# Optimization experiments

Hardware: AMD Instinct MI355X
Metric: run time of the kernel (lower is better)

The kernel has to match this reference:

```python
import jax, jax.numpy as jnp
import numpy as np

N = 50000       # nodes
E = 800000      # edges (before self-loops)
G = 512         # graphs in batch
IN = 128        # in_channels
HID = 256       # hidden_channels
HEADS = 8
CH = HID // HEADS
NEG_SLOPE = 0.2 # GATConv leaky relu slope
BN_EPS = 1e-5
OUT_CLASSES = [3, 3]


def setup_inputs() -> dict:
    key = jax.random.key(0)
    ks = iter(jax.random.split(key, 64))
    inp = {}
    inp["x"] = jax.random.normal(next(ks), (N, IN), jnp.float32)
    inp["edge_index"] = jax.random.randint(next(ks), (2, E), 0, N)
    inp["batch"] = jnp.sort(jax.random.randint(next(ks), (N,), 0, G))
    dims = [IN, HID, HID]
    for l, d in enumerate(dims, start=1):
        inp[f"W{l}"] = jax.random.normal(next(ks), (d, HID), jnp.float32) / np.float32(np.sqrt(d))
        inp[f"as{l}"] = jax.random.normal(next(ks), (HEADS, CH), jnp.float32) * 0.1
        inp[f"ad{l}"] = jax.random.normal(next(ks), (HEADS, CH), jnp.float32) * 0.1
        inp[f"b{l}"] = jnp.zeros((HID,), jnp.float32)
        inp[f"g{l}"] = 1.0 + 0.1 * jax.random.normal(next(ks), (HID,), jnp.float32)
        inp[f"be{l}"] = 0.1 * jax.random.normal(next(ks), (HID,), jnp.float32)
        inp[f"m{l}"] = 0.1 * jax.random.normal(next(ks), (HID,), jnp.float32)
        inp[f"v{l}"] = 0.5 + jax.random.uniform(next(ks), (HID,), jnp.float32)
    for i, c in enumerate(OUT_CLASSES):
        inp[f"ow{i}"] = jax.random.normal(next(ks), (3 * HID, c), jnp.float32) / np.float32(np.sqrt(3 * HID))
        inp[f"ob{i}"] = jnp.zeros((c,), jnp.float32)
    return inp


def gat_conv(x, W, a_src, a_dst, bias, src, dst):
    # x: [N, D] -> h: [N, H, C]
    h = (x @ W).reshape(N, HEADS, CH)
    s_src = jnp.sum(h * a_src, axis=-1)           # [N, H]
    s_dst = jnp.sum(h * a_dst, axis=-1)           # [N, H]
    alpha = jax.nn.leaky_relu(s_src[src] + s_dst[dst], NEG_SLOPE)  # [E', H]
    # segment softmax over incoming edges of each destination node
    mx = jax.ops.segment_max(alpha, dst, num_segments=N)           # [N, H]
    e = jnp.exp(alpha - mx[dst])
    Z = jax.ops.segment_sum(e, dst, num_segments=N)                # [N, H]
    coef = e / (Z[dst] + 1e-16)                                    # [E', H]
    msg = h[src] * coef[:, :, None]                                # [E', H, C]
    out = jax.ops.segment_sum(msg, dst, num_segments=N)            # [N, H, C]
    return out.reshape(N, HID) + bias


def batch_norm(h, g, b, m, v):
    return (h - m) * jax.lax.rsqrt(v + BN_EPS) * g + b


def reference(x, edge_index, batch,
              W1, as1, ad1, b1, g1, be1, m1, v1,
              W2, as2, ad2, b2, g2, be2, m2, v2,
              W3, as3, ad3, b3, g3, be3, m3, v3,
              ow0, ob0, ow1, ob1):
    # GATConv adds self-loops by default
    loop = jnp.arange(N, dtype=edge_index.dtype)
    src = jnp.concatenate([edge_index[0], loop])
    dst = jnp.concatenate([edge_index[1], loop])

    h = jax.nn.elu(batch_norm(gat_conv(x, W1, as1, ad1, b1, src, dst), g1, be1, m1, v1))
    h = jax.nn.elu(batch_norm(gat_conv(h, W2, as2, ad2, b2, src, dst), g2, be2, m2, v2) + h)
    h = jax.nn.elu(batch_norm(gat_conv(h, W3, as3, ad3, b3, src, dst), g3, be3, m3, v3) + h)

    sums = jax.ops.segment_sum(h, batch, num_segments=G)                       # add pool
    cnt = jax.ops.segment_sum(jnp.ones((N, 1), h.dtype), batch, num_segments=G)
    mean = sums / jnp.maximum(cnt, 1.0)                                        # mean pool
    mx = jax.ops.segment_max(h, batch, num_segments=G)                         # max pool
    mx = jnp.where(jnp.isfinite(mx), mx, 0.0)
    pooled = jnp.concatenate([mean, sums, mx], axis=1)                         # [G, 3*HID]

    return (pooled @ ow0 + ob0, pooled @ ow1 + ob1)
```

## Files before the change

kernel.cpp:

```cpp
#include <hip/hip_runtime.h>
#include <hip/hip_bf16.h>
#include <math.h>

#define N_NODES 50000
#define N_EDGES 800000
#define EP (N_EDGES + N_NODES)
#define G_GRAPHS 512
#define HID 256
#define HEADS 8
#define NEG_SLOPE 0.2f
#define BN_EPS 1e-5f
#define NB_SCAN ((N_NODES + 1023) / 1024)

typedef __attribute__((ext_vector_type(8))) short short8;
typedef __attribute__((ext_vector_type(8))) unsigned short ushort8v;
typedef __attribute__((ext_vector_type(4))) float floatx4;

__device__ __forceinline__ float bf2f(ushort u) {
    return __uint_as_float(((unsigned)u) << 16);
}
__device__ __forceinline__ ushort f2bf(float f) {
    unsigned u = __float_as_uint(f);
    u += 0x7fff + ((u >> 16) & 1);
    return (ushort)(u >> 16);
}


__global__ void hist_kernel(const int* __restrict__ ei, int* __restrict__ fill) {
    int e = blockIdx.x * 256 + threadIdx.x;
    if (e >= EP) return;
    int d = (e < N_EDGES) ? ei[N_EDGES + e] : (e - N_EDGES);
    atomicAdd(&fill[d], 1);
}

__global__ void scan1_kernel(const int* __restrict__ fill, int* __restrict__ rowptr,
                             int* __restrict__ bsum) {
    __shared__ int sdata[1024];
    int tid = threadIdx.x;
    int idx = blockIdx.x * 1024 + tid;
    int v = (idx < N_NODES) ? fill[idx] : 0;
    sdata[tid] = v;
    __syncthreads();
    for (int off = 1; off < 1024; off <<= 1) {
        int x = (tid >= off) ? sdata[tid - off] : 0;
        __syncthreads();
        sdata[tid] += x;
        __syncthreads();
    }
    if (idx < N_NODES) rowptr[idx] = sdata[tid] - v;
    if (tid == 1023) bsum[blockIdx.x] = sdata[1023];
}

__global__ void scan3_kernel(int* __restrict__ rowptr, int* __restrict__ fill,
                             const int* __restrict__ bsum) {
    __shared__ int soff[2];
    int tid = threadIdx.x;
    if (tid < 64) {
        int v = (tid < NB_SCAN) ? bsum[tid] : 0;
        int incl = v;
#pragma unroll
        for (int off = 1; off < 64; off <<= 1) {
            int x = __shfl_up(incl, off, 64);
            if (tid >= off) incl += x;
        }
        if (tid == blockIdx.x) soff[0] = incl - v;
        if (tid == NB_SCAN - 1) soff[1] = incl;
    }
    __syncthreads();
    int idx = blockIdx.x * 1024 + tid;
    if (idx < N_NODES) {
        int e = rowptr[idx] + soff[0];
        rowptr[idx] = e;
        fill[idx] = e;
    }
    if (idx == N_NODES) rowptr[N_NODES] = soff[1];
}

__global__ void scatter_kernel(const int* __restrict__ ei, int* __restrict__ fill,
                               int* __restrict__ esrc) {
    int e = blockIdx.x * 256 + threadIdx.x;
    if (e >= EP) return;
    int s, d;
    if (e < N_EDGES) { s = ei[e]; d = ei[N_EDGES + e]; }
    else             { s = d = e - N_EDGES; }
    int pos = atomicAdd(&fill[d], 1);
    esrc[pos] = s;
}

__global__ void gstart_kernel(const int* __restrict__ batch, int* __restrict__ gstart) {
    int g = blockIdx.x * 64 + threadIdx.x;
    if (g > G_GRAPHS) return;
    int lo = 0, hi = N_NODES;
    while (lo < hi) { int mid = (lo + hi) >> 1; if (batch[mid] < g) lo = mid + 1; else hi = mid; }
    gstart[g] = lo;
}


__global__ void cvt_kernel(const float* __restrict__ in, ushort* __restrict__ out, int n4) {
    int i = blockIdx.x * 256 + threadIdx.x;
    if (i >= n4) return;
    float4 v = *(const float4*)&in[(size_t)i * 4];
    ushort4 o = {f2bf(v.x), f2bf(v.y), f2bf(v.z), f2bf(v.w)};
    *(ushort4*)&out[(size_t)i * 4] = o;
}

__global__ void wt_all_kernel(const float* __restrict__ W0, const float* __restrict__ W1,
                              const float* __restrict__ W2, ushort* __restrict__ Wt0,
                              ushort* __restrict__ Wt1, ushort* __restrict__ Wt2) {
    int m = blockIdx.y;
    const float* W = (m == 0) ? W0 : (m == 1) ? W1 : W2;
    ushort* Wt = (m == 0) ? Wt0 : (m == 1) ? Wt1 : Wt2;
    int K = (m == 0) ? 128 : 256;
    int c = blockIdx.x, k = threadIdx.x;
    if (k < K) Wt[(size_t)c * K + k] = f2bf(W[(size_t)k * HID + c]);
}

#define BM 128
#define BN 128
#define BK 64

__global__ __launch_bounds__(256) void gemm_kernel(
    const ushort* __restrict__ A, const ushort* __restrict__ Bt,
    ushort* __restrict__ C, int M, int K)
{
    __shared__ __align__(16) char As[2][BM * BK * 2];
    __shared__ __align__(16) char Bs[2][BN * BK * 2];

    int t = threadIdx.x;
    int w = t >> 6, lane = t & 63;
    int bm = blockIdx.x * BM, bn = blockIdx.y * BN;
    int wr = (w >> 1) * 64, wc = (w & 1) * 64;

    floatx4 acc[4][4] = {};

    int l8 = lane >> 3;
    int cb = ((lane & 7) << 4) ^ ((l8 & 7) << 4);
    int rsw = (lane & 7) << 4;
    int nt = K / BK;

    auto stage = [&](int buf, int k0) {
#pragma unroll
        for (int c = 0; c < 4; c++) {
            int q = w * 4 + c;
            int row = q * 8 + l8;
            int ar = bm + row; if (ar > M - 1) ar = M - 1;
            const char* src = (const char*)A + ((size_t)ar * K + k0) * 2 + cb;
            __builtin_amdgcn_global_load_lds(
                (const __attribute__((address_space(1))) void*)src,
                (__attribute__((address_space(3))) void*)&As[buf][q * 1024], 16, 0, 0);
            int br = bn + row;
            const char* srcb = (const char*)Bt + ((size_t)br * K + k0) * 2 + cb;
            __builtin_amdgcn_global_load_lds(
                (const __attribute__((address_space(1))) void*)srcb,
                (__attribute__((address_space(3))) void*)&Bs[buf][q * 1024], 16, 0, 0);
        }
    };

    stage(0, 0);
    for (int tt = 0; tt < nt; tt++) {
        int cur = tt & 1;
        __builtin_amdgcn_s_barrier();
        if (tt + 1 < nt) {
            stage(cur ^ 1, (tt + 1) * BK);
            asm volatile("s_waitcnt vmcnt(8)" ::: "memory");
        } else {
            asm volatile("s_waitcnt vmcnt(0)" ::: "memory");
        }
        __builtin_amdgcn_sched_barrier(0);
        __builtin_amdgcn_s_barrier();
        __builtin_amdgcn_sched_barrier(0);

        const char* asb = As[cur];
        const char* bsb = Bs[cur];
#pragma unroll
        for (int ks = 0; ks < 2; ks++) {
            int kb = ks * 64 + ((lane >> 4) << 4);
            short8 a[4], b[4];
#pragma unroll
            for (int m = 0; m < 4; m++) {
                int row = wr + m * 16 + (lane & 15);
                a[m] = *(const short8*)&asb[row * 128 + (kb ^ rsw)];
            }
#pragma unroll
            for (int n = 0; n < 4; n++) {
                int row = wc + n * 16 + (lane & 15);
                b[n] = *(const short8*)&bsb[row * 128 + (kb ^ rsw)];
            }
#pragma unroll
            for (int m = 0; m < 4; m++)
#pragma unroll
                for (int n = 0; n < 4; n++)
                    acc[m][n] = __builtin_amdgcn_mfma_f32_16x16x32_bf16(a[m], b[n], acc[m][n], 0, 0, 0);
        }
    }

    int cl = lane & 15, rh = lane >> 4;
#pragma unroll
    for (int m = 0; m < 4; m++) {
#pragma unroll
        for (int r = 0; r < 4; r++) {
            int row = bm + wr + m * 16 + rh * 4 + r;
            if (row < M) {
                size_t base = (size_t)row * HID + bn + wc;
#pragma unroll
                for (int n = 0; n < 4; n++)
                    C[base + n * 16 + cl] = f2bf(acc[m][n][r]);
            }
        }
    }
}

__global__ __launch_bounds__(256) void score_kernel(
    const ushort* __restrict__ hb, const float* __restrict__ asrc,
    const float* __restrict__ adst, float* __restrict__ ssrc,
    float* __restrict__ sdst) {
    int t = threadIdx.x;
    int lane = t & 63;
    int wid = t >> 6;
    unsigned n = (unsigned)(blockIdx.x * 8 + wid * 2 + (lane >> 5));
    unsigned cl = lane & 31;
    unsigned c0 = cl * 8u;
    ushort8v hv = *(const ushort8v*)&hb[n * 256u + c0];
    float s1 = 0.f, s2 = 0.f;
#pragma unroll
    for (int j = 0; j < 8; j++) {
        float v = bf2f(hv[j]);
        s1 += v * asrc[c0 + j];
        s2 += v * adst[c0 + j];
    }
    s1 += __shfl_xor(s1, 1, 64); s2 += __shfl_xor(s2, 1, 64);
    s1 += __shfl_xor(s1, 2, 64); s2 += __shfl_xor(s2, 2, 64);
    if ((cl & 3) == 0) {
        unsigned h = cl >> 2;
        ssrc[n * 8u + h] = s1;
        sdst[n * 8u + h] = s2;
    }
}

__global__ __launch_bounds__(256) void agg_kernel(
    const ushort* __restrict__ hb, const float* __restrict__ ssrc,
    const float* __restrict__ sdst, const int* __restrict__ rowptr,
    const int* __restrict__ esrc, const float* __restrict__ bias,
    const float* __restrict__ gam, const float* __restrict__ bet,
    const float* __restrict__ bmean, const float* __restrict__ bvar,
    const ushort* __restrict__ residb, ushort* __restrict__ outb) {
    int wid = threadIdx.x >> 6;
    int lane = threadIdx.x & 63;
    int n = blockIdx.x * 4 + wid;
    if (n >= N_NODES) return;
    int start = rowptr[n], end = rowptr[n + 1];
    int slot = lane >> 5;
    unsigned cl = lane & 31;
    unsigned c0 = cl * 8u;
    unsigned head = cl >> 2;
    float sdh = sdst[(unsigned)n * 8u + head];

    float z = 0.f;
    float acc[8] = {};
    int i = start + slot;
    for (; i + 6 < end; i += 8) {
        unsigned s0 = (unsigned)esrc[i], s1 = (unsigned)esrc[i + 2];
        unsigned s2 = (unsigned)esrc[i + 4], s3 = (unsigned)esrc[i + 6];
        float a0 = ssrc[s0 * 8u + head] + sdh;
        float a1 = ssrc[s1 * 8u + head] + sdh;
        float a2 = ssrc[s2 * 8u + head] + sdh;
        float a3 = ssrc[s3 * 8u + head] + sdh;
        ushort8v h0 = *(const ushort8v*)&hb[s0 * 256u + c0];
        ushort8v h1 = *(const ushort8v*)&hb[s1 * 256u + c0];
        ushort8v h2 = *(const ushort8v*)&hb[s2 * 256u + c0];
        ushort8v h3 = *(const ushort8v*)&hb[s3 * 256u + c0];
        a0 = fmaxf(a0, NEG_SLOPE * a0);
        a1 = fmaxf(a1, NEG_SLOPE * a1);
        a2 = fmaxf(a2, NEG_SLOPE * a2);
        a3 = fmaxf(a3, NEG_SLOPE * a3);
        float e0 = __expf(a0), e1 = __expf(a1), e2 = __expf(a2), e3 = __expf(a3);
        z += (e0 + e1) + (e2 + e3);
#pragma unroll
        for (int j = 0; j < 8; j++)
            acc[j] += (e0 * bf2f(h0[j]) + e1 * bf2f(h1[j])) +
                      (e2 * bf2f(h2[j]) + e3 * bf2f(h3[j]));
    }
    for (; i < end; i += 2) {
        unsigned s = (unsigned)esrc[i];
        float a = ssrc[s * 8u + head] + sdh;
        a = fmaxf(a, NEG_SLOPE * a);
        float e = __expf(a);
        ushort8v hv = *(const ushort8v*)&hb[s * 256u + c0];
        z += e;
#pragma unroll
        for (int j = 0; j < 8; j++)
            acc[j] += e * bf2f(hv[j]);
    }
    z += __shfl_xor(z, 32, 64);
#pragma unroll
    for (int j = 0; j < 8; j++)
        acc[j] += __shfl_xor(acc[j], 32, 64);

    if (lane < 32) {
        float inv = 1.f / (z + 1e-16f);
        float4 bv0 = *(const float4*)&bias[c0],   bv1 = *(const float4*)&bias[c0 + 4];
        float4 gv0 = *(const float4*)&gam[c0],    gv1 = *(const float4*)&gam[c0 + 4];
        float4 be0 = *(const float4*)&bet[c0],    be1 = *(const float4*)&bet[c0 + 4];
        float4 mv0 = *(const float4*)&bmean[c0],  mv1 = *(const float4*)&bmean[c0 + 4];
        float4 vv0 = *(const float4*)&bvar[c0],   vv1 = *(const float4*)&bvar[c0 + 4];
        float bs[8] = {bv0.x, bv0.y, bv0.z, bv0.w, bv1.x, bv1.y, bv1.z, bv1.w};
        float gs[8] = {gv0.x, gv0.y, gv0.z, gv0.w, gv1.x, gv1.y, gv1.z, gv1.w};
        float bes[8] = {be0.x, be0.y, be0.z, be0.w, be1.x, be1.y, be1.z, be1.w};
        float ms[8] = {mv0.x, mv0.y, mv0.z, mv0.w, mv1.x, mv1.y, mv1.z, mv1.w};
        float vs[8] = {vv0.x, vv0.y, vv0.z, vv0.w, vv1.x, vv1.y, vv1.z, vv1.w};
        float rs[8] = {};
        if (residb) {
            ushort8v rv = *(const ushort8v*)&residb[(unsigned)n * 256u + c0];
#pragma unroll
            for (int j = 0; j < 8; j++) rs[j] = bf2f(rv[j]);
        }
        ushort8v ob;
#pragma unroll
        for (int j = 0; j < 8; j++) {
            float val = acc[j] * inv + bs[j];
            val = (val - ms[j]) * rsqrtf(vs[j] + BN_EPS) * gs[j] + bes[j];
            val += rs[j];
            val = (val > 0.f) ? val : expm1f(val);
            ob[j] = f2bf(val);
        }
        *(ushort8v*)&outb[(unsigned)n * 256u + c0] = ob;
    }
}

__global__ void poolhead_kernel(const ushort* __restrict__ hbf, const int* __restrict__ gstart,
                                const float* __restrict__ ow0, const float* __restrict__ ob0,
                                const float* __restrict__ ow1, const float* __restrict__ ob1,
                                float* __restrict__ out) {
    int g = blockIdx.x;
    int t = threadIdx.x;
    int s = gstart[g], e = gstart[g + 1];
    float sum = 0.f, mx = -INFINITY;
    for (int n = s; n < e; n++) {
        float v = bf2f(hbf[(unsigned)n * 256u + t]);
        sum += v;
        mx = fmaxf(mx, v);
    }
    int cnt = e - s;
    float mean = sum / fmaxf((float)cnt, 1.f);
    if (cnt == 0) mx = 0.f;

    float a0[3], a1[3];
#pragma unroll
    for (int j = 0; j < 3; j++) {
        a0[j] = mean * ow0[t * 3 + j] + sum * ow0[(256 + t) * 3 + j] + mx * ow0[(512 + t) * 3 + j];
        a1[j] = mean * ow1[t * 3 + j] + sum * ow1[(256 + t) * 3 + j] + mx * ow1[(512 + t) * 3 + j];
    }
    __shared__ float sd[6][256];
#pragma unroll
    for (int j = 0; j < 3; j++) { sd[j][t] = a0[j]; sd[3 + j][t] = a1[j]; }
    __syncthreads();
    for (int off = 128; off; off >>= 1) {
        if (t < off) {
#pragma unroll
            for (int j = 0; j < 6; j++) sd[j][t] += sd[j][t + off];
        }
        __syncthreads();
    }
    if (t < 3) {
        out[g * 3 + t] = sd[t][0] + ob0[t];
        out[1536 + g * 3 + t] = sd[3 + t][0] + ob1[t];
    }
}

extern "C" void kernel_launch(void* const* d_in, const int* in_sizes, int n_in,
                              void* d_out, int out_size, void* d_ws, size_t ws_size,
                              hipStream_t stream) {
    const float* x     = (const float*)d_in[0];
    const int*   ei    = (const int*)d_in[1];
    const int*   batch = (const int*)d_in[2];
    const float* W[3]  = {(const float*)d_in[3], (const float*)d_in[11], (const float*)d_in[19]};
    const float* AS[3] = {(const float*)d_in[4], (const float*)d_in[12], (const float*)d_in[20]};
    const float* AD[3] = {(const float*)d_in[5], (const float*)d_in[13], (const float*)d_in[21]};
    const float* B[3]  = {(const float*)d_in[6], (const float*)d_in[14], (const float*)d_in[22]};
    const float* GM[3] = {(const float*)d_in[7], (const float*)d_in[15], (const float*)d_in[23]};
    const float* BE[3] = {(const float*)d_in[8], (const float*)d_in[16], (const float*)d_in[24]};
    const float* M[3]  = {(const float*)d_in[9], (const float*)d_in[17], (const float*)d_in[25]};
    const float* V[3]  = {(const float*)d_in[10], (const float*)d_in[18], (const float*)d_in[26]};
    const float* ow0 = (const float*)d_in[27];
    const float* ob0 = (const float*)d_in[28];
    const float* ow1 = (const float*)d_in[29];
    const float* ob1 = (const float*)d_in[30];
    float* out = (float*)d_out;

    char* p = (char*)d_ws;
    int* rowptr = (int*)p;  p += (size_t)(N_NODES + 1) * 4;
    int* fill   = (int*)p;  p += (size_t)N_NODES * 4;
    int* esrc   = (int*)p;  p += (size_t)EP * 4;
    int* gstart = (int*)p;  p += (size_t)(G_GRAPHS + 1) * 4;
    int* bsum   = (int*)p;  p += (size_t)(NB_SCAN + 1) * 4;
    p = (char*)(((uintptr_t)p + 255) & ~(uintptr_t)255);
    ushort* hb    = (ushort*)p; p += (size_t)N_NODES * HID * 2;
    ushort* curhb = (ushort*)p; p += (size_t)N_NODES * HID * 2;
    ushort* xb    = (ushort*)p; p += (size_t)N_NODES * 128 * 2;
    ushort* Wt0   = (ushort*)p; p += (size_t)256 * 128 * 2;
    ushort* Wt1   = (ushort*)p; p += (size_t)256 * 256 * 2;
    ushort* Wt2   = (ushort*)p; p += (size_t)256 * 256 * 2;
    float* ssrc   = (float*)p;  p += (size_t)N_NODES * HEADS * 4;
    float* sdst   = (float*)p;  p += (size_t)N_NODES * HEADS * 4;

    hipMemsetAsync(fill, 0, (size_t)N_NODES * 4, stream);
    hist_kernel<<<(EP + 255) / 256, 256, 0, stream>>>(ei, fill);
    scan1_kernel<<<NB_SCAN, 1024, 0, stream>>>(fill, rowptr, bsum);
    scan3_kernel<<<NB_SCAN, 1024, 0, stream>>>(rowptr, fill, bsum);
    scatter_kernel<<<(EP + 255) / 256, 256, 0, stream>>>(ei, fill, esrc);
    gstart_kernel<<<(G_GRAPHS + 64) / 64, 64, 0, stream>>>(batch, gstart);

    cvt_kernel<<<(N_NODES * 128 / 4 + 255) / 256, 256, 0, stream>>>(x, xb, N_NODES * 128 / 4);
    {
        dim3 wgrid(256, 3);
        wt_all_kernel<<<wgrid, 256, 0, stream>>>(W[0], W[1], W[2], Wt0, Wt1, Wt2);
    }
    const ushort* Wt[3] = {Wt0, Wt1, Wt2};

    dim3 ggrid((N_NODES + BM - 1) / BM, HID / BN);
    int sgrid = N_NODES / 8;
    int agrid = (N_NODES + 3) / 4;

    gemm_kernel<<<ggrid, 256, 0, stream>>>(xb, Wt[0], hb, N_NODES, 128);
    score_kernel<<<sgrid, 256, 0, stream>>>(hb, AS[0], AD[0], ssrc, sdst);
    agg_kernel<<<agrid, 256, 0, stream>>>(hb, ssrc, sdst, rowptr, esrc,
                                          B[0], GM[0], BE[0], M[0], V[0],
                                          nullptr, curhb);
    for (int l = 1; l < 3; l++) {
        gemm_kernel<<<ggrid, 256, 0, stream>>>(curhb, Wt[l], hb, N_NODES, 256);
        score_kernel<<<sgrid, 256, 0, stream>>>(hb, AS[l], AD[l], ssrc, sdst);
        agg_kernel<<<agrid, 256, 0, stream>>>(hb, ssrc, sdst, rowptr, esrc,
                                              B[l], GM[l], BE[l], M[l], V[l],
                                              curhb, curhb);
    }

    poolhead_kernel<<<G_GRAPHS, 256, 0, stream>>>(curhb, gstart, ow0, ob0, ow1, ob1, out);
}
```

Before: 561.4 us.

## Fuse attention scores into GEMM epilogue and merge preprocessing kernels

Computes the per-head source and destination attention scores inside the GEMM epilogue from fp32 accumulators. Partial dot products are reduced with wave shuffles and atomically added into zeroed per-layer score buffers, which removes the separate score kernel and its re-read of h. Also merges the bf16 conversion, weight transpose, degree histogram and graph-start search into one launch. In exchange it adds atomics, a larger memset, and scores taken from fp32 rather than bf16-rounded values.

Measured after the change: 646.3 us. 15.1% more time.

```diff
diff --git a/kernel.cpp b/kernel.cpp
--- a/kernel.cpp
+++ b/kernel.cpp
@@ -12,6 +12,12 @@
 #define BN_EPS 1e-5f
 #define NB_SCAN ((N_NODES + 1023) / 1024)
 
+#define NB_CVT 6250
+#define NB_WT  256
+#define NB_HIST ((EP + 255) / 256)
+#define NB_GST 3
+#define NB_PREP (NB_CVT + NB_WT + NB_HIST + NB_GST)
+
 typedef __attribute__((ext_vector_type(8))) short short8;
 typedef __attribute__((ext_vector_type(8))) unsigned short ushort8v;
 typedef __attribute__((ext_vector_type(4))) float floatx4;
@@ -25,12 +31,39 @@
     return (ushort)(u >> 16);
 }
 
-
-__global__ void hist_kernel(const int* __restrict__ ei, int* __restrict__ fill) {
-    int e = blockIdx.x * 256 + threadIdx.x;
-    if (e >= EP) return;
-    int d = (e < N_EDGES) ? ei[N_EDGES + e] : (e - N_EDGES);
-    atomicAdd(&fill[d], 1);
+__global__ __launch_bounds__(256) void prep_kernel(
+    const float* __restrict__ x, ushort* __restrict__ xb,
+    const float* __restrict__ W0, const float* __restrict__ W1,
+    const float* __restrict__ W2, ushort* __restrict__ Wt0,
+    ushort* __restrict__ Wt1, ushort* __restrict__ Wt2,
+    const int* __restrict__ ei, int* __restrict__ fill,
+    const int* __restrict__ batch, int* __restrict__ gstart) {
+    int b = blockIdx.x;
+    int tid = threadIdx.x;
+    if (b < NB_CVT) {
+        int i = b * 256 + tid;
+        float4 v = *(const float4*)&x[(size_t)i * 4];
+        ushort4 o = {f2bf(v.x), f2bf(v.y), f2bf(v.z), f2bf(v.w)};
+        *(ushort4*)&xb[(size_t)i * 4] = o;
+    } else if (b < NB_CVT + NB_WT) {
+        int c = b - NB_CVT;
+        if (tid < 128) Wt0[c * 128 + tid] = f2bf(W0[(size_t)tid * HID + c]);
+        Wt1[c * 256 + tid] = f2bf(W1[(size_t)tid * HID + c]);
+        Wt2[c * 256 + tid] = f2bf(W2[(size_t)tid * HID + c]);
+    } else if (b < NB_CVT + NB_WT + NB_HIST) {
+        int e = (b - NB_CVT - NB_WT) * 256 + tid;
+        if (e < EP) {
+            int d = (e < N_EDGES) ? ei[N_EDGES + e] : (e - N_EDGES);
+            atomicAdd(&fill[d], 1);
+        }
+    } else {
+        int g = (b - NB_CVT - NB_WT - NB_HIST) * 256 + tid;
+        if (g <= G_GRAPHS) {
+            int lo = 0, hi = N_NODES;
+            while (lo < hi) { int mid = (lo + hi) >> 1; if (batch[mid] < g) lo = mid + 1; else hi = mid; }
+            gstart[g] = lo;
+        }
+    }
 }
 
 __global__ void scan1_kernel(const int* __restrict__ fill, int* __restrict__ rowptr,
@@ -87,41 +120,15 @@
     esrc[pos] = s;
 }
 
-__global__ void gstart_kernel(const int* __restrict__ batch, int* __restrict__ gstart) {
-    int g = blockIdx.x * 64 + threadIdx.x;
-    if (g > G_GRAPHS) return;
-    int lo = 0, hi = N_NODES;
-    while (lo < hi) { int mid = (lo + hi) >> 1; if (batch[mid] < g) lo = mid + 1; else hi = mid; }
-    gstart[g] = lo;
-}
-
-
-__global__ void cvt_kernel(const float* __restrict__ in, ushort* __restrict__ out, int n4) {
-    int i = blockIdx.x * 256 + threadIdx.x;
-    if (i >= n4) return;
-    float4 v = *(const float4*)&in[(size_t)i * 4];
-    ushort4 o = {f2bf(v.x), f2bf(v.y), f2bf(v.z), f2bf(v.w)};
-    *(ushort4*)&out[(size_t)i * 4] = o;
-}
-
-__global__ void wt_all_kernel(const float* __restrict__ W0, const float* __restrict__ W1,
-                              const float* __restrict__ W2, ushort* __restrict__ Wt0,
-                              ushort* __restrict__ Wt1, ushort* __restrict__ Wt2) {
-    int m = blockIdx.y;
-    const float* W = (m == 0) ? W0 : (m == 1) ? W1 : W2;
-    ushort* Wt = (m == 0) ? Wt0 : (m == 1) ? Wt1 : Wt2;
-    int K = (m == 0) ? 128 : 256;
-    int c = blockIdx.x, k = threadIdx.x;
-    if (k < K) Wt[(size_t)c * K + k] = f2bf(W[(size_t)k * HID + c]);
-}
-
 #define BM 128
 #define BN 128
 #define BK 64
 
 __global__ __launch_bounds__(256) void gemm_kernel(
     const ushort* __restrict__ A, const ushort* __restrict__ Bt,
-    ushort* __restrict__ C, int M, int K)
+    ushort* __restrict__ C, int M, int K,
+    const float* __restrict__ asf, const float* __restrict__ adf,
+    float* __restrict__ ssrc, float* __restrict__ sdst)
 {
     __shared__ __align__(16) char As[2][BM * BK * 2];
     __shared__ __align__(16) char Bs[2][BN * BK * 2];
@@ -208,32 +215,38 @@
             }
         }
     }
-}
-
-__global__ __launch_bounds__(256) void score_kernel(
-    const ushort* __restrict__ hb, const float* __restrict__ asrc,
-    const float* __restrict__ adst, float* __restrict__ ssrc,
-    float* __restrict__ sdst) {
-    int t = threadIdx.x;
-    int lane = t & 63;
-    int wid = t >> 6;
-    unsigned n = (unsigned)(blockIdx.x * 8 + wid * 2 + (lane >> 5));
-    unsigned cl = lane & 31;
-    unsigned c0 = cl * 8u;
-    ushort8v hv = *(const ushort8v*)&hb[n * 256u + c0];
-    float s1 = 0.f, s2 = 0.f;
-#pragma unroll
-    for (int j = 0; j < 8; j++) {
-        float v = bf2f(hv[j]);
-        s1 += v * asrc[c0 + j];
-        s2 += v * adst[c0 + j];
-    }
-    s1 += __shfl_xor(s1, 1, 64); s2 += __shfl_xor(s2, 1, 64);
-    s1 += __shfl_xor(s1, 2, 64); s2 += __shfl_xor(s2, 2, 64);
-    if ((cl & 3) == 0) {
-        unsigned h = cl >> 2;
-        ssrc[n * 8u + h] = s1;
-        sdst[n * 8u + h] = s2;
+
+    int base_c = bn + wc;
+    float av[4], dv[4];
+#pragma unroll
+    for (int n = 0; n < 4; n++) {
+        av[n] = asf[base_c + n * 16 + cl];
+        dv[n] = adf[base_c + n * 16 + cl];
+    }
+    int headA = base_c >> 5, headB = headA + 1;
+#pragma unroll
+    for (int m = 0; m < 4; m++) {
+#pragma unroll
+        for (int r = 0; r < 4; r++) {
+            int row = bm + wr + m * 16 + rh * 4 + r;
+            float psA = acc[m][0][r] * av[0] + acc[m][1][r] * av[1];
+            float psB = acc[m][2][r] * av[2] + acc[m][3][r] * av[3];
+            float pdA = acc[m][0][r] * dv[0] + acc[m][1][r] * dv[1];
+            float pdB = acc[m][2][r] * dv[2] + acc[m][3][r] * dv[3];
+#pragma unroll
+            for (int off = 1; off < 16; off <<= 1) {
+                psA += __shfl_xor(psA, off, 64);
+                psB += __shfl_xor(psB, off, 64);
+                pdA += __shfl_xor(pdA, off, 64);
+                pdB += __shfl_xor(pdB, off, 64);
+            }
+            if (cl == 0 && row < M) {
+                atomicAdd(&ssrc[(unsigned)row * 8u + headA], psA);
+                atomicAdd(&ssrc[(unsigned)row * 8u + headB], psB);
+                atomicAdd(&sdst[(unsigned)row * 8u + headA], pdA);
+                atomicAdd(&sdst[(unsigned)row * 8u + headB], pdB);
+            }
+        }
     }
 }
 
@@ -388,8 +401,14 @@
     float* out = (float*)d_out;
 
     char* p = (char*)d_ws;
+    int* fill   = (int*)p;  p += (size_t)N_NODES * 4;
+    float* sc[3][2];
+    for (int l = 0; l < 3; l++) {
+        sc[l][0] = (float*)p; p += (size_t)N_NODES * HEADS * 4;
+        sc[l][1] = (float*)p; p += (size_t)N_NODES * HEADS * 4;
+    }
+    size_t zero_bytes = (size_t)p - (size_t)d_ws;
     int* rowptr = (int*)p;  p += (size_t)(N_NODES + 1) * 4;
-    int* fill   = (int*)p;  p += (size_t)N_NODES * 4;
     int* esrc   = (int*)p;  p += (size_t)EP * 4;
     int* gstart = (int*)p;  p += (size_t)(G_GRAPHS + 1) * 4;
     int* bsum   = (int*)p;  p += (size_t)(NB_SCAN + 1) * 4;
@@ -400,36 +419,28 @@
     ushort* Wt0   = (ushort*)p; p += (size_t)256 * 128 * 2;
     ushort* Wt1   = (ushort*)p; p += (size_t)256 * 256 * 2;
     ushort* Wt2   = (ushort*)p; p += (size_t)256 * 256 * 2;
-    float* ssrc   = (float*)p;  p += (size_t)N_NODES * HEADS * 4;
-    float* sdst   = (float*)p;  p += (size_t)N_NODES * HEADS * 4;
-
-    hipMemsetAsync(fill, 0, (size_t)N_NODES * 4, stream);
-    hist_kernel<<<(EP + 255) / 256, 256, 0, stream>>>(ei, fill);
+
+    hipMemsetAsync(d_ws, 0, zero_bytes, stream);
+
+    prep_kernel<<<NB_PREP, 256, 0, stream>>>(x, xb, W[0], W[1], W[2], Wt0, Wt1, Wt2,
+                                             ei, fill, batch, gstart);
     scan1_kernel<<<NB_SCAN, 1024, 0, stream>>>(fill, rowptr, bsum);
     scan3_kernel<<<NB_SCAN, 1024, 0, stream>>>(rowptr, fill, bsum);
     scatter_kernel<<<(EP + 255) / 256, 256, 0, stream>>>(ei, fill, esrc);
-    gstart_kernel<<<(G_GRAPHS + 64) / 64, 64, 0, stream>>>(batch, gstart);
-
-    cvt_kernel<<<(N_NODES * 128 / 4 + 255) / 256, 256, 0, stream>>>(x, xb, N_NODES * 128 / 4);
-    {
-        dim3 wgrid(256, 3);
-        wt_all_kernel<<<wgrid, 256, 0, stream>>>(W[0], W[1], W[2], Wt0, Wt1, Wt2);
-    }
+
     const ushort* Wt[3] = {Wt0, Wt1, Wt2};
-
     dim3 ggrid((N_NODES + BM - 1) / BM, HID / BN);
-    int sgrid = N_NODES / 8;
     int agrid = (N_NODES + 3) / 4;
 
-    gemm_kernel<<<ggrid, 256, 0, stream>>>(xb, Wt[0], hb, N_NODES, 128);
-    score_kernel<<<sgrid, 256, 0, stream>>>(hb, AS[0], AD[0], ssrc, sdst);
-    agg_kernel<<<agrid, 256, 0, stream>>>(hb, ssrc, sdst, rowptr, esrc,
+    gemm_kernel<<<ggrid, 256, 0, stream>>>(xb, Wt[0], hb, N_NODES, 128,
+                                           AS[0], AD[0], sc[0][0], sc[0][1]);
+    agg_kernel<<<agrid, 256, 0, stream>>>(hb, sc[0][0], sc[0][1], rowptr, esrc,
                                           B[0], GM[0], BE[0], M[0], V[0],
                                           nullptr, curhb);
     for (int l = 1; l < 3; l++) {
-        gemm_kernel<<<ggrid, 256, 0, stream>>>(curhb, Wt[l], hb, N_NODES, 256);
-        score_kernel<<<sgrid, 256, 0, stream>>>(hb, AS[l], AD[l], ssrc, sdst);
-        agg_kernel<<<agrid, 256, 0, stream>>>(hb, ssrc, sdst, rowptr, esrc,
+        gemm_kernel<<<ggrid, 256, 0, stream>>>(curhb, Wt[l], hb, N_NODES, 256,
+                                               AS[l], AD[l], sc[l][0], sc[l][1]);
+        agg_kernel<<<agrid, 256, 0, stream>>>(hb, sc[l][0], sc[l][1], rowptr, esrc,
                                               B[l], GM[l], BE[l], M[l], V[l],
                                               curhb, curhb);
     }
```
